# Kernel tuning notes

Hardware: AMD Instinct MI355X
Metric: run time of the kernel (lower is better)

Reference implementation:

```python
import jax, jax.numpy as jnp
import numpy as np

T, B, A_DIM = 64, 128, 5
N_AGENTS, N_CAP = 8, 7
OBS_D = 64
CAP_D = N_AGENTS * N_CAP  # 56
FC, HN, TGT = 128, 128, 64
D = N_CAP + 1  # transformer model dim = 8
NH, FF, NL = 4, 64, 2
EPS = 1e-6


def _ln(x, s, b):
    m = jnp.mean(x, -1, keepdims=True)
    v = jnp.mean(jnp.square(x - m), -1, keepdims=True)
    return (x - m) * jax.lax.rsqrt(v + EPS) * s + b


def _hyper(x, w1, b1, w2, b2):
    return jax.nn.relu(x @ w1 + b1) @ w2 + b2


def setup_inputs() -> dict:
    key = jax.random.key(0)
    ks = iter(jax.random.split(key, 40))

    def rn(shape, s=0.1):
        return jax.random.normal(next(ks), shape, jnp.float32) * s

    return dict(
        hidden=jnp.zeros((B, FC), jnp.float32),
        full_obs=jax.random.normal(next(ks), (T, B, OBS_D + CAP_D), jnp.float32),
        dones=jax.random.randint(next(ks), (T, B), 0, 2, jnp.int32),
        embed_w=rn((OBS_D, FC)), embed_b=jnp.zeros((FC,), jnp.float32),
        gru_wi=rn((FC, 3 * FC)), gru_wh=rn((FC, 3 * FC)), gru_bh=jnp.zeros((3 * FC,), jnp.float32),
        tWq=rn((NL, D, D), 0.3), tWk=rn((NL, D, D), 0.3), tWv=rn((NL, D, D), 0.3), tWo=rn((NL, D, D), 0.3),
        ln1_s=jnp.ones((NL, D), jnp.float32), ln1_b=jnp.zeros((NL, D), jnp.float32),
        ffw1=rn((NL, D, FF), 0.2), ffb1=jnp.zeros((NL, FF), jnp.float32),
        ffw2=rn((NL, FF, D), 0.2), ffb2=jnp.zeros((NL, D), jnp.float32),
        ln2_s=jnp.ones((NL, D), jnp.float32), ln2_b=jnp.zeros((NL, D), jnp.float32),
        hw1_1=rn((D, HN)), hb1_1=jnp.zeros((HN,), jnp.float32), hw2_1=rn((HN, FC * TGT), 0.02), hb2_1=jnp.zeros((FC * TGT,), jnp.float32),
        hw1_2=rn((D, HN)), hb1_2=jnp.zeros((HN,), jnp.float32), hw2_2=rn((HN, TGT), 0.02), hb2_2=jnp.zeros((TGT,), jnp.float32),
        hw1_3=rn((D, HN)), hb1_3=jnp.zeros((HN,), jnp.float32), hw2_3=rn((HN, TGT * A_DIM), 0.01), hb2_3=jnp.zeros((TGT * A_DIM,), jnp.float32),
        hw1_4=rn((D, HN)), hb1_4=jnp.zeros((HN,), jnp.float32), hw2_4=rn((HN, A_DIM), 0.01), hb2_4=jnp.zeros((A_DIM,), jnp.float32),
    )


def reference(hidden, full_obs, dones, embed_w, embed_b, gru_wi, gru_wh, gru_bh,
              tWq, tWk, tWv, tWo, ln1_s, ln1_b, ffw1, ffb1, ffw2, ffb2, ln2_s, ln2_b,
              hw1_1, hb1_1, hw2_1, hb2_1, hw1_2, hb1_2, hw2_2, hb2_2,
              hw1_3, hb1_3, hw2_3, hb2_3, hw1_4, hb1_4, hw2_4, hb2_4):
    obs = full_obs[:, :, :OBS_D]          # [T,B,OBS_D]
    cap = full_obs[:, :, OBS_D:]          # [T,B,CAP_D]
    emb = jax.nn.relu(obs @ embed_w + embed_b)  # [T,B,FC]
    resets = dones.astype(bool)

    # --- GRU scan over time (flax GRUCell math: input dense no bias, hidden dense with bias) ---
    def gru_step(h, xt):
        e, d = xt
        h = jnp.where(d[:, None], 0.0, h)
        gi = e @ gru_wi                   # [B, 3*FC]
        gh = h @ gru_wh + gru_bh
        ir, iz, inn = jnp.split(gi, 3, -1)
        hr, hz, hn = jnp.split(gh, 3, -1)
        r = jax.nn.sigmoid(ir + hr)
        z = jax.nn.sigmoid(iz + hz)
        n = jnp.tanh(inn + r * hn)
        hnew = (1.0 - z) * n + z * h
        return hnew, hnew

    hidden, emb_seq = jax.lax.scan(gru_step, hidden, (emb, resets))

    # --- transformer over agents dim ---
    x = cap.reshape(T * B, N_AGENTS, N_CAP)
    flag = jnp.zeros((T * B, N_AGENTS, 1), jnp.float32).at[:, 0, 0].set(1.0)
    x = jnp.concatenate([x, flag], axis=-1)   # [N, A, D]
    hd = D // NH
    scale = 1.0 / jnp.sqrt(jnp.float32(hd))
    for l in range(NL):
        q = (x @ tWq[l]).reshape(-1, N_AGENTS, NH, hd)
        k = (x @ tWk[l]).reshape(-1, N_AGENTS, NH, hd)
        v = (x @ tWv[l]).reshape(-1, N_AGENTS, NH, hd)
        att = jax.nn.softmax(jnp.einsum('nqhd,nkhd->nhqk', q, k) * scale, axis=-1)
        o = jnp.einsum('nhqk,nkhd->nqhd', att, v).reshape(-1, N_AGENTS, D) @ tWo[l]
        # original does x = norm(attn + x); x = x + dropout(x) -> doubles x
        x = 2.0 * _ln(o + x, ln1_s[l], ln1_b[l])
        ff = jax.nn.relu(x @ ffw1[l] + ffb1[l]) @ ffw2[l] + ffb2[l]
        x = 2.0 * _ln(ff + x, ln2_s[l], ln2_b[l])
    cap_repr = jnp.mean(x, axis=1).reshape(T, B, D)

    # --- hypernetworks -> per-(t,b) weights ---
    w1 = _hyper(cap_repr, hw1_1, hb1_1, hw2_1, hb2_1).reshape(T, B, FC, TGT)
    b1 = _hyper(cap_repr, hw1_2, hb1_2, hw2_2, hb2_2).reshape(T, B, 1, TGT)
    w2 = _hyper(cap_repr, hw1_3, hb1_3, hw2_3, hb2_3).reshape(T, B, TGT, A_DIM)
    b2 = _hyper(cap_repr, hw1_4, hb1_4, hw2_4, hb2_4).reshape(T, B, 1, A_DIM)

    h1 = jax.nn.relu(emb_seq[:, :, None, :] @ w1 + b1)   # [T,B,1,TGT]
    logits = (h1 @ w2 + b2).squeeze(2)                    # [T,B,A_DIM]
    return hidden, logits
```

## Files before the change

### kernel.cpp

```cpp
#include <hip/hip_runtime.h>
#include <hip/hip_bf16.h>
#include <stdint.h>

#define TT 64
#define BB 128
#define OBSD 64
#define FOBS 120
#define FC 128
#define G3 384
#define NS 8192
#define DD 8
#define FF 64
#define HN 128
#define TGT 64
#define ADIM 5

typedef __attribute__((ext_vector_type(8))) short bf16x8;
typedef __attribute__((ext_vector_type(4))) float f32x4;

__device__ __forceinline__ float sigmoidf_(float x) { return 1.0f / (1.0f + __expf(-x)); }
__device__ __forceinline__ float tanhf_(float x) {
    float e = __expf(-2.0f * fabsf(x));
    float r = (1.0f - e) / (1.0f + e);
    return copysignf(r, x);
}
__device__ __forceinline__ unsigned short f2bf_rne(float x) {
    unsigned u = __float_as_uint(x);
    return (unsigned short)((u + 0x7fffu + ((u >> 16) & 1u)) >> 16);
}

__global__ __launch_bounds__(256) void k_embed(
    const float* __restrict__ fobs, const float* __restrict__ We,
    const float* __restrict__ be, float* __restrict__ emb)
{
    __shared__ float obs_t[64][68];
    __shared__ float W_t[64][128];
    int tid = threadIdx.x;
    int s0 = blockIdx.x * 64;
    {
        int rl = tid >> 4, e4 = tid & 15;
#pragma unroll
        for (int rr = 0; rr < 4; ++rr) {
            int r = rl + rr * 16;
            float4 v = *(const float4*)&fobs[(size_t)(s0 + r) * FOBS + e4 * 4];
            *(float4*)&obs_t[r][e4 * 4] = v;
        }
    }
#pragma unroll
    for (int i = 0; i < 8; ++i) {
        int idx = tid + i * 256;
        int e = idx >> 5, c4 = idx & 31;
        float4 v = *(const float4*)&We[(size_t)e * 128 + c4 * 4];
        *(float4*)&W_t[e][c4 * 4] = v;
    }
    __syncthreads();
    int c = tid & 127, half = tid >> 7;
    float acc[32];
    float bc = be[c];
#pragma unroll
    for (int k = 0; k < 32; ++k) acc[k] = bc;
#pragma unroll
    for (int e4 = 0; e4 < 16; ++e4) {
        float w0 = W_t[4 * e4 + 0][c], w1 = W_t[4 * e4 + 1][c];
        float w2 = W_t[4 * e4 + 2][c], w3 = W_t[4 * e4 + 3][c];
#pragma unroll
        for (int k = 0; k < 32; ++k) {
            float4 ov = *(const float4*)&obs_t[half * 32 + k][e4 * 4];
            acc[k] += ov.x * w0 + ov.y * w1 + ov.z * w2 + ov.w * w3;
        }
    }
#pragma unroll
    for (int k = 0; k < 32; ++k)
        emb[(size_t)(s0 + half * 32 + k) * FC + c] = fmaxf(acc[k], 0.0f);
}

__global__ __launch_bounds__(256) void k_gi(
    const float* __restrict__ emb, const float* __restrict__ Wi, float* __restrict__ gi)
{
    __shared__ float e_t[64][132];
    __shared__ float w_t[128 * 64];
    int tid = threadIdx.x;
    int st = blockIdx.x / 6, gt = blockIdx.x % 6;
    int s0 = st * 64, g0 = gt * 64;
#pragma unroll
    for (int i = 0; i < 8; ++i) {
        int idx = tid + i * 256;
        int r = idx >> 5, c4 = idx & 31;
        float4 v = *(const float4*)&emb[(size_t)(s0 + r) * FC + c4 * 4];
        *(float4*)&e_t[r][c4 * 4] = v;
    }
#pragma unroll
    for (int i = 0; i < 8; ++i) {
        int idx = tid + i * 256;
        int r = idx >> 4, g4 = idx & 15;
        float4 v = *(const float4*)&Wi[(size_t)r * G3 + g0 + g4 * 4];
        *(float4*)&w_t[r * 64 + g4 * 4] = v;
    }
    __syncthreads();
    int sb4 = (tid >> 4) * 4, ob4 = (tid & 15) * 4;
    float acc[4][4];
#pragma unroll
    for (int a = 0; a < 4; ++a)
#pragma unroll
        for (int b = 0; b < 4; ++b) acc[a][b] = 0.0f;
    for (int c4 = 0; c4 < 32; ++c4) {
        float4 e4[4], w4[4];
#pragma unroll
        for (int si = 0; si < 4; ++si) e4[si] = *(const float4*)&e_t[sb4 + si][c4 * 4];
#pragma unroll
        for (int cc = 0; cc < 4; ++cc) w4[cc] = *(const float4*)&w_t[(c4 * 4 + cc) * 64 + ob4];
#pragma unroll
        for (int si = 0; si < 4; ++si) {
            const float* ep = (const float*)&e4[si];
#pragma unroll
            for (int cc = 0; cc < 4; ++cc) {
                float ev = ep[cc];
                const float* wp = (const float*)&w4[cc];
                acc[si][0] += ev * wp[0];
                acc[si][1] += ev * wp[1];
                acc[si][2] += ev * wp[2];
                acc[si][3] += ev * wp[3];
            }
        }
    }
#pragma unroll
    for (int si = 0; si < 4; ++si) {
        float4 sv;
        sv.x = acc[si][0]; sv.y = acc[si][1]; sv.z = acc[si][2]; sv.w = acc[si][3];
        *(float4*)&gi[(size_t)(s0 + sb4 + si) * G3 + g0 + ob4] = sv;
    }
}

__global__ __launch_bounds__(256) void k_prepW(
    const float* __restrict__ W, unsigned short* __restrict__ W_swz)
{
    int fid = blockIdx.x * 256 + threadIdx.x;
    int lane = fid & 63;
    int ks = (fid >> 6) & 3;
    int j  = (fid >> 8) & 127;
    int nt = (fid >> 15);
    int col = nt * 16 + (lane & 15);
    int kbase = ks * 32 + ((lane >> 4) * 8);
    const float* src = W + ((size_t)j * 128 + kbase) * 64 + col;
    unsigned short o[8];
#pragma unroll
    for (int i = 0; i < 8; ++i) o[i] = f2bf_rne(src[(size_t)i * 64]);
    size_t slot = ((size_t)((nt * 128 + j) * 4 + ks)) * 64 + lane;
    *(uint4*)&W_swz[slot * 8] = *(const uint4*)o;
}

__global__ __launch_bounds__(512, 2) void k_gru(
    const float* __restrict__ gi, const float* __restrict__ Wh, const float* __restrict__ bh,
    const int* __restrict__ dones, const float* __restrict__ h0,
    float* __restrict__ emb_seq, unsigned short* __restrict__ embb,
    float* __restrict__ hid_out)
{
    __shared__ float h_lds[2][144];
    int b = blockIdx.x, tid = threadIdx.x;
    int c = tid >> 2, q = tid & 3;
    int posc = (c >> 5) * 36 + (c & 31);

    float W[96];
#pragma unroll
    for (int g = 0; g < 3; ++g)
#pragma unroll
        for (int i = 0; i < 32; ++i)
            W[g * 32 + i] = Wh[(size_t)(q * 32 + i) * G3 + g * 128 + c];
    float bq0 = bh[c], bq1 = bh[128 + c], bq2 = bh[256 + c];

    if (tid < 128) h_lds[0][(tid >> 5) * 36 + (tid & 31)] = h0[(size_t)b * FC + tid];

    const float* g0p = gi + ((size_t)0 * BB + b) * G3;
    const float* g1p = gi + ((size_t)1 * BB + b) * G3;
    float gc0 = g0p[c], gc1 = g0p[128 + c], gc2 = g0p[256 + c];
    float n10 = g1p[c], n11 = g1p[128 + c], n12 = g1p[256 + c];
    int dval = dones[b];
    int dn1 = dones[BB + b];
    __syncthreads();

    int cur = 0;
    for (int t = 0; t < TT; ++t) {
        int t2 = (t + 2 < TT) ? t + 2 : TT - 1;
        const float* gp2 = gi + ((size_t)t2 * BB + b) * G3;
        float p0 = gp2[c], p1 = gp2[128 + c], p2 = gp2[256 + c];
        int pd = dones[t2 * BB + b];

        float d0 = 0.f, d1 = 0.f, d2 = 0.f;
        const float* hb = &h_lds[cur][q * 36];
#pragma unroll
        for (int i4 = 0; i4 < 8; ++i4) {
            float4 h4 = *(const float4*)&hb[i4 * 4];
            const float* hp = (const float*)&h4;
#pragma unroll
            for (int e = 0; e < 4; ++e) {
                int i = i4 * 4 + e;
                d0 += W[i] * hp[e];
                d1 += W[32 + i] * hp[e];
                d2 += W[64 + i] * hp[e];
            }
        }
        d0 += __shfl_xor(d0, 1, 64); d0 += __shfl_xor(d0, 2, 64);
        d1 += __shfl_xor(d1, 1, 64); d1 += __shfl_xor(d1, 2, 64);
        d2 += __shfl_xor(d2, 1, 64); d2 += __shfl_xor(d2, 2, 64);

        float hs = dval ? 0.0f : 1.0f;
        float hold = h_lds[cur][posc];
        float r = sigmoidf_(gc0 + d0 * hs + bq0);
        float z = sigmoidf_(gc1 + d1 * hs + bq1);
        float n = tanhf_(gc2 + r * (d2 * hs + bq2));
        float hnew = (1.0f - z) * n + z * (hs * hold);

        if (q == 0) {
            h_lds[cur ^ 1][posc] = hnew;
            emb_seq[((size_t)t * BB + b) * FC + c] = hnew;
            embb[((size_t)t * BB + b) * FC + c] = f2bf_rne(hnew);
        }
        gc0 = n10; gc1 = n11; gc2 = n12;
        n10 = p0;  n11 = p1;  n12 = p2;
        dval = dn1; dn1 = pd;
        __syncthreads();
        cur ^= 1;
    }
    if (tid < 128) hid_out[(size_t)b * FC + tid] = h_lds[cur][(tid >> 5) * 36 + (tid & 31)];
}

__global__ __launch_bounds__(256) void k_attn(
    const float* __restrict__ fobs,
    const float* __restrict__ tWq, const float* __restrict__ tWk,
    const float* __restrict__ tWv, const float* __restrict__ tWo,
    const float* __restrict__ ln1s, const float* __restrict__ ln1b,
    const float* __restrict__ ffw1, const float* __restrict__ ffb1,
    const float* __restrict__ ffw2, const float* __restrict__ ffb2,
    const float* __restrict__ ln2s, const float* __restrict__ ln2b,
    float* __restrict__ cap_repr)
{
    __shared__ float wq[2][8][8], wk[2][8][8], wv[2][8][8], wo[2][8][8];
    __shared__ float l1s[2][8], l1b[2][8], l2s[2][8], l2b[2][8];
    __shared__ float f1[2][8][64], fb1[2][64];
    __shared__ float f2[2][64][8], fb2w[2][8];
    __shared__ float k_l[32][8][9], v_l[32][8][9];
    int tid = threadIdx.x;
    for (int i = tid; i < 128; i += 256) {
        ((float*)wq)[i] = tWq[i]; ((float*)wk)[i] = tWk[i];
        ((float*)wv)[i] = tWv[i]; ((float*)wo)[i] = tWo[i];
        ((float*)fb1)[i] = ffb1[i];
    }
    if (tid < 16) {
        ((float*)l1s)[tid] = ln1s[tid]; ((float*)l1b)[tid] = ln1b[tid];
        ((float*)l2s)[tid] = ln2s[tid]; ((float*)l2b)[tid] = ln2b[tid];
        ((float*)fb2w)[tid] = ffb2[tid];
    }
    for (int i = tid; i < 1024; i += 256) { ((float*)f1)[i] = ffw1[i]; ((float*)f2)[i] = ffw2[i]; }
    int sl = tid >> 3, a = tid & 7;
    int s = blockIdx.x * 32 + sl;
    float x[8];
#pragma unroll
    for (int i = 0; i < 7; ++i) x[i] = fobs[(size_t)s * FOBS + OBSD + a * 7 + i];
    x[7] = (a == 0) ? 1.0f : 0.0f;
    __syncthreads();
    for (int l = 0; l < 2; ++l) {
        float q[8], k[8], v[8];
#pragma unroll
        for (int d = 0; d < 8; ++d) { q[d] = 0.f; k[d] = 0.f; v[d] = 0.f; }
#pragma unroll
        for (int e = 0; e < 8; ++e) {
            float xe = x[e];
#pragma unroll
            for (int d = 0; d < 8; ++d) {
                q[d] += xe * wq[l][e][d];
                k[d] += xe * wk[l][e][d];
                v[d] += xe * wv[l][e][d];
            }
        }
#pragma unroll
        for (int d = 0; d < 8; ++d) { k_l[sl][a][d] = k[d]; v_l[sl][a][d] = v[d]; }
        __syncthreads();
        float o[8];
#pragma unroll
        for (int h = 0; h < 4; ++h) {
            float sc[8]; float mx = -1e30f;
#pragma unroll
            for (int ka = 0; ka < 8; ++ka) {
                float sv = (q[2 * h] * k_l[sl][ka][2 * h] + q[2 * h + 1] * k_l[sl][ka][2 * h + 1])
                           * 0.70710678118654752f;
                sc[ka] = sv; mx = fmaxf(mx, sv);
            }
            float ssum = 0.f;
#pragma unroll
            for (int ka = 0; ka < 8; ++ka) { sc[ka] = __expf(sc[ka] - mx); ssum += sc[ka]; }
            float inv = 1.0f / ssum;
            float o0 = 0.f, o1 = 0.f;
#pragma unroll
            for (int ka = 0; ka < 8; ++ka) {
                float at = sc[ka] * inv;
                o0 += at * v_l[sl][ka][2 * h];
                o1 += at * v_l[sl][ka][2 * h + 1];
            }
            o[2 * h] = o0; o[2 * h + 1] = o1;
        }
        float y[8];
#pragma unroll
        for (int e = 0; e < 8; ++e) y[e] = x[e];
#pragma unroll
        for (int d = 0; d < 8; ++d) {
            float od = o[d];
#pragma unroll
            for (int e = 0; e < 8; ++e) y[e] += od * wo[l][d][e];
        }
        {
            float m = 0.f;
#pragma unroll
            for (int e = 0; e < 8; ++e) m += y[e];
            m *= 0.125f;
            float vv = 0.f;
#pragma unroll
            for (int e = 0; e < 8; ++e) { float dd = y[e] - m; vv += dd * dd; }
            vv *= 0.125f;
            float rs = rsqrtf(vv + 1e-6f);
#pragma unroll
            for (int e = 0; e < 8; ++e)
                x[e] = 2.0f * ((y[e] - m) * rs * l1s[l][e] + l1b[l][e]);
        }
        float t1[64];
#pragma unroll
        for (int f = 0; f < 64; ++f) t1[f] = 0.f;
#pragma unroll
        for (int e = 0; e < 8; ++e) {
            float xe = x[e];
#pragma unroll
            for (int f = 0; f < 64; ++f) t1[f] += xe * f1[l][e][f];
        }
        float y2[8];
#pragma unroll
        for (int e = 0; e < 8; ++e) y2[e] = x[e] + fb2w[l][e];
#pragma unroll
        for (int f = 0; f < 64; ++f) {
            float tf = fmaxf(t1[f] + fb1[l][f], 0.0f);
#pragma unroll
            for (int e = 0; e < 8; ++e) y2[e] += tf * f2[l][f][e];
        }
        {
            float m = 0.f;
#pragma unroll
            for (int e = 0; e < 8; ++e) m += y2[e];
            m *= 0.125f;
            float vv = 0.f;
#pragma unroll
            for (int e = 0; e < 8; ++e) { float dd = y2[e] - m; vv += dd * dd; }
            vv *= 0.125f;
            float rs = rsqrtf(vv + 1e-6f);
#pragma unroll
            for (int e = 0; e < 8; ++e)
                x[e] = 2.0f * ((y2[e] - m) * rs * l2s[l][e] + l2b[l][e]);
        }
        __syncthreads();
    }
#pragma unroll
    for (int e = 0; e < 8; ++e) {
        float xv = x[e];
        xv += __shfl_xor(xv, 1, 8);
        xv += __shfl_xor(xv, 2, 8);
        xv += __shfl_xor(xv, 4, 8);
        if (a == 0) cap_repr[(size_t)s * 8 + e] = xv * 0.125f;
    }
}

__global__ __launch_bounds__(256) void k_hyper(
    const float* __restrict__ cap_repr, const float* __restrict__ emb_seq,
    const float* __restrict__ hw1_1, const float* __restrict__ hb1_1,
    const float* __restrict__ hw1_2, const float* __restrict__ hb1_2,
    const float* __restrict__ hw1_3, const float* __restrict__ hb1_3,
    const float* __restrict__ hw1_4, const float* __restrict__ hb1_4,
    const float* __restrict__ hb2_1,
    const float* __restrict__ hw2_2, const float* __restrict__ hb2_2,
    const float* __restrict__ hw2_3, const float* __restrict__ hb2_3,
    const float* __restrict__ hw2_4, const float* __restrict__ hb2_4,
    float* __restrict__ hh1g, float* __restrict__ b1eff,
    float* __restrict__ w2h, float* __restrict__ b2h)
{
    __shared__ float cr[16][8];
    __shared__ float hh[4][16][132];
    __shared__ float es[16][132];
    int tid = threadIdx.x;
    int s0 = blockIdx.x * 16;
    if (tid < 128) ((float*)cr)[tid] = cap_repr[(size_t)s0 * 8 + tid];
#pragma unroll
    for (int i = 0; i < 2; ++i) {
        int idx = tid + i * 256;
        int r = idx >> 5, c4 = idx & 31;
        float4 v = *(const float4*)&emb_seq[(size_t)(s0 + r) * FC + c4 * 4];
        *(float4*)&es[r][c4 * 4] = v;
    }
    __syncthreads();
#pragma unroll
    for (int it = 0; it < 32; ++it) {
        int idx = tid + it * 256;
        int u = idx & 127;
        int sn = (idx >> 7) & 15;
        int n = idx >> 11;
        const float* w = (n == 0) ? hw1_1 : ((n == 1) ? hw1_2 : ((n == 2) ? hw1_3 : hw1_4));
        const float* bb = (n == 0) ? hb1_1 : ((n == 1) ? hb1_2 : ((n == 2) ? hb1_3 : hb1_4));
        float acc = bb[u];
#pragma unroll
        for (int e = 0; e < 8; ++e) acc += cr[sn][e] * w[e * 128 + u];
        acc = fmaxf(acc, 0.0f);
        hh[n][sn][u] = acc;
        if (n == 0) hh1g[(size_t)(s0 + sn) * 128 + u] = acc;
    }
    __syncthreads();
#pragma unroll
    for (int it = 0; it < 4; ++it) {
        int idx = tid + it * 256;
        int o = idx & 63, sn = idx >> 6;
        float acc = hb2_2[o];
        for (int j = 0; j < 128; ++j) acc += hh[1][sn][j] * hw2_2[j * 64 + o];
        for (int c = 0; c < 128; ++c) acc += es[sn][c] * hb2_1[c * 64 + o];
        b1eff[(size_t)(s0 + sn) * 64 + o] = acc;
    }
    for (int it = 0; it < 2; ++it) {
        int oa = tid + it * 256;
        if (oa < 320) {
            float acc[16];
#pragma unroll
            for (int sn = 0; sn < 16; ++sn) acc[sn] = 0.f;
            for (int j = 0; j < 128; ++j) {
                float w = hw2_3[j * 320 + oa];
#pragma unroll
                for (int sn = 0; sn < 16; ++sn) acc[sn] += hh[2][sn][j] * w;
            }
            float bb = hb2_3[oa];
#pragma unroll
            for (int sn = 0; sn < 16; ++sn) w2h[(size_t)(s0 + sn) * 320 + oa] = acc[sn] + bb;
        }
    }
    if (tid < 80) {
        int aa = tid % 5, sn = tid / 5;
        float acc = hb2_4[aa];
        for (int j = 0; j < 128; ++j) acc += hh[3][sn][j] * hw2_4[j * 5 + aa];
        b2h[(size_t)(s0 + sn) * 5 + aa] = acc;
    }
}

__global__ __launch_bounds__(256) void k_bigmm_mfma(
    const unsigned short* __restrict__ embb, const float* __restrict__ hh1g,
    const unsigned short* __restrict__ W_swz, float* __restrict__ partials)
{
    __shared__ float hh1T[32][68];
    int tid = threadIdx.x;
    int nt = tid >> 6, lane = tid & 63;
    int mt = blockIdx.x >> 2, ksp = blockIdx.x & 3;
    int s0 = mt * 64, j0 = ksp * 32;

#pragma unroll
    for (int it = 0; it < 8; ++it) {
        int idx = tid + it * 256;
        int r = idx >> 5, jj = idx & 31;
        hh1T[jj][r] = hh1g[(size_t)(s0 + r) * 128 + j0 + jj];
    }

    bf16x8 emb_r[4][4];
    int rrow = lane & 15;
    int cbase = (lane >> 4) * 8;
#pragma unroll
    for (int rt = 0; rt < 4; ++rt)
#pragma unroll
        for (int ks = 0; ks < 4; ++ks)
            emb_r[rt][ks] = *(const bf16x8*)&embb[(size_t)(s0 + rt * 16 + rrow) * 128 + ks * 32 + cbase];

    const bf16x8* Wg = (const bf16x8*)W_swz + ((size_t)(nt * 128 + j0) * 4) * 64 + lane;
    bf16x8 bf[4][4];
#pragma unroll
    for (int s = 0; s < 4; ++s)
#pragma unroll
        for (int q = 0; q < 4; ++q) bf[s][q] = Wg[(size_t)s * 256 + q * 64];

    f32x4 acc[4];
#pragma unroll
    for (int rt = 0; rt < 4; ++rt) acc[rt] = (f32x4){0.f, 0.f, 0.f, 0.f};

    int hrow = 4 * (lane >> 4);
    __syncthreads();

    for (int jj = 0; jj < 32; jj += 4) {
#pragma unroll
        for (int s = 0; s < 4; ++s) {
            int j = jj + s;
            f32x4 P[4];
#pragma unroll
            for (int rt = 0; rt < 4; ++rt) P[rt] = (f32x4){0.f, 0.f, 0.f, 0.f};
#pragma unroll
            for (int ks = 0; ks < 4; ++ks) {
                bf16x8 b = bf[s][ks];
#pragma unroll
                for (int rt = 0; rt < 4; ++rt)
                    P[rt] = __builtin_amdgcn_mfma_f32_16x16x32_bf16(emb_r[rt][ks], b, P[rt], 0, 0, 0);
            }
            if (j + 4 < 32) {
#pragma unroll
                for (int q = 0; q < 4; ++q) bf[s][q] = Wg[(size_t)(j + 4) * 256 + q * 64];
            }
            const float* hp = &hh1T[j][hrow];
#pragma unroll
            for (int rt = 0; rt < 4; ++rt) {
                float4 h4 = *(const float4*)&hp[rt * 16];
                const float* hv = (const float*)&h4;
#pragma unroll
                for (int r = 0; r < 4; ++r) acc[rt][r] += hv[r] * P[rt][r];
            }
        }
    }
    float* pb = partials + (size_t)ksp * (NS * 64);
    int colg = nt * 16 + (lane & 15);
#pragma unroll
    for (int rt = 0; rt < 4; ++rt) {
#pragma unroll
        for (int r = 0; r < 4; ++r) {
            int rowg = s0 + rt * 16 + hrow + r;
            pb[(size_t)rowg * 64 + colg] = acc[rt][r];
        }
    }
}

__global__ __launch_bounds__(256) void k_final(
    const float* __restrict__ partials, const float* __restrict__ b1eff,
    const float* __restrict__ w2h, const float* __restrict__ b2h, float* __restrict__ out)
{
    int tid = threadIdx.x;
    int wv = tid >> 6, lane = tid & 63;
    int s = blockIdx.x * 4 + wv;
    float h1 = b1eff[(size_t)s * 64 + lane];
#pragma unroll
    for (int ks = 0; ks < 4; ++ks) h1 += partials[(size_t)ks * (NS * 64) + (size_t)s * 64 + lane];
    h1 = fmaxf(h1, 0.0f);
    float lg[5];
#pragma unroll
    for (int aa = 0; aa < 5; ++aa) lg[aa] = h1 * w2h[(size_t)s * 320 + lane * 5 + aa];
#pragma unroll
    for (int off = 32; off >= 1; off >>= 1) {
#pragma unroll
        for (int aa = 0; aa < 5; ++aa) lg[aa] += __shfl_xor(lg[aa], off, 64);
    }
    if (lane == 0) {
#pragma unroll
        for (int aa = 0; aa < 5; ++aa)
            out[16384 + (size_t)s * 5 + aa] = lg[aa] + b2h[(size_t)s * 5 + aa];
    }
}

extern "C" void kernel_launch(void* const* d_in, const int* in_sizes, int n_in,
                              void* d_out, int out_size, void* d_ws, size_t ws_size,
                              hipStream_t stream)
{
    (void)in_sizes; (void)n_in; (void)out_size; (void)ws_size;
    const float* hidden  = (const float*)d_in[0];
    const float* fobs    = (const float*)d_in[1];
    const int*   dones   = (const int*)d_in[2];
    const float* embed_w = (const float*)d_in[3];
    const float* embed_b = (const float*)d_in[4];
    const float* gru_wi  = (const float*)d_in[5];
    const float* gru_wh  = (const float*)d_in[6];
    const float* gru_bh  = (const float*)d_in[7];
    const float* tWq  = (const float*)d_in[8];
    const float* tWk  = (const float*)d_in[9];
    const float* tWv  = (const float*)d_in[10];
    const float* tWo  = (const float*)d_in[11];
    const float* ln1s = (const float*)d_in[12];
    const float* ln1b = (const float*)d_in[13];
    const float* ffw1 = (const float*)d_in[14];
    const float* ffb1 = (const float*)d_in[15];
    const float* ffw2 = (const float*)d_in[16];
    const float* ffb2 = (const float*)d_in[17];
    const float* ln2s = (const float*)d_in[18];
    const float* ln2b = (const float*)d_in[19];
    const float* hw1_1 = (const float*)d_in[20]; const float* hb1_1 = (const float*)d_in[21];
    const float* hw2_1 = (const float*)d_in[22]; const float* hb2_1 = (const float*)d_in[23];
    const float* hw1_2 = (const float*)d_in[24]; const float* hb1_2 = (const float*)d_in[25];
    const float* hw2_2 = (const float*)d_in[26]; const float* hb2_2 = (const float*)d_in[27];
    const float* hw1_3 = (const float*)d_in[28]; const float* hb1_3 = (const float*)d_in[29];
    const float* hw2_3 = (const float*)d_in[30]; const float* hb2_3 = (const float*)d_in[31];
    const float* hw1_4 = (const float*)d_in[32]; const float* hb1_4 = (const float*)d_in[33];
    const float* hw2_4 = (const float*)d_in[34]; const float* hb2_4 = (const float*)d_in[35];
    float* out = (float*)d_out;
    float* ws  = (float*)d_ws;

    float* gi      = ws;
    float* parts   = ws;
    float* emb     = gi      + 3145728;
    unsigned short* W_swz    = (unsigned short*)emb;
    unsigned short* emb_bf16 = (unsigned short*)(emb + 524288);
    float* emb_seq = emb     + 1048576;
    float* cap_rep = emb_seq + 1048576;
    float* hh1g    = cap_rep + 65536;
    float* b1eff_  = hh1g    + 1048576;
    float* w2hb    = b1eff_  + 524288;
    float* b2hb    = w2hb    + 2621440;

    k_embed<<<128, 256, 0, stream>>>(fobs, embed_w, embed_b, emb);
    k_gi<<<768, 256, 0, stream>>>(emb, gru_wi, gi);
    k_prepW<<<512, 256, 0, stream>>>(hw2_1, W_swz);
    k_gru<<<128, 512, 0, stream>>>(gi, gru_wh, gru_bh, dones, hidden, emb_seq, emb_bf16, out);
    k_attn<<<256, 256, 0, stream>>>(fobs, tWq, tWk, tWv, tWo, ln1s, ln1b,
                                    ffw1, ffb1, ffw2, ffb2, ln2s, ln2b, cap_rep);
    k_hyper<<<512, 256, 0, stream>>>(cap_rep, emb_seq,
                                     hw1_1, hb1_1, hw1_2, hb1_2, hw1_3, hb1_3, hw1_4, hb1_4,
                                     hb2_1, hw2_2, hb2_2, hw2_3, hb2_3, hw2_4, hb2_4,
                                     hh1g, b1eff_, w2hb, b2hb);
    k_bigmm_mfma<<<512, 256, 0, stream>>>(emb_bf16, hh1g, W_swz, parts);
    k_final<<<2048, 256, 0, stream>>>(parts, b1eff_, w2hb, b2hb, out);
}
```

Baseline: 463.4 us.

## Split big MFMA kernel rows across 8 waves to cut register pressure

The bf16 MFMA kernel now uses 512 threads per block, and each wave covers 32 rows of the 64-row tile instead of all 64. This halves the per-wave embedding and accumulator registers and shrinks the weight prefetch buffer from four j-steps to two. The aim is to raise occupancy and latency hiding through more resident waves. In exchange each W fragment is loaded by two waves, so global or L2 traffic for weights doubles, and each wave has less prefetch depth.

Result: faster. 441.8 us (-4.7%).

```diff
diff --git a/kernel.cpp b/kernel.cpp
--- a/kernel.cpp
+++ b/kernel.cpp
@@ -441,84 +441,101 @@
     }
 }
 
-__global__ __launch_bounds__(256) void k_bigmm_mfma(
+__global__ __launch_bounds__(512, 3) void k_bigmm_mfma(
     const unsigned short* __restrict__ embb, const float* __restrict__ hh1g,
     const unsigned short* __restrict__ W_swz, float* __restrict__ partials)
 {
     __shared__ float hh1T[32][68];
     int tid = threadIdx.x;
-    int nt = tid >> 6, lane = tid & 63;
+    int w = tid >> 6, lane = tid & 63;
+    int nt = w & 3, rh = w >> 2;
     int mt = blockIdx.x >> 2, ksp = blockIdx.x & 3;
     int s0 = mt * 64, j0 = ksp * 32;
 
 #pragma unroll
-    for (int it = 0; it < 8; ++it) {
-        int idx = tid + it * 256;
+    for (int it = 0; it < 4; ++it) {
+        int idx = tid + it * 512;
         int r = idx >> 5, jj = idx & 31;
         hh1T[jj][r] = hh1g[(size_t)(s0 + r) * 128 + j0 + jj];
     }
 
-    bf16x8 emb_r[4][4];
-    int rrow = lane & 15;
+    bf16x8 emb_r[2][4];
+    int rrow = rh * 32 + (lane & 15);
     int cbase = (lane >> 4) * 8;
 #pragma unroll
-    for (int rt = 0; rt < 4; ++rt)
+    for (int rt = 0; rt < 2; ++rt)
 #pragma unroll
         for (int ks = 0; ks < 4; ++ks)
-            emb_r[rt][ks] = *(const bf16x8*)&embb[(size_t)(s0 + rt * 16 + rrow) * 128 + ks * 32 + cbase];
+            emb_r[rt][ks] = *(const bf16x8*)&embb[(size_t)(s0 + rrow + rt * 16) * 128 + ks * 32 + cbase];
 
     const bf16x8* Wg = (const bf16x8*)W_swz + ((size_t)(nt * 128 + j0) * 4) * 64 + lane;
-    bf16x8 bf[4][4];
-#pragma unroll
-    for (int s = 0; s < 4; ++s)
-#pragma unroll
-        for (int q = 0; q < 4; ++q) bf[s][q] = Wg[(size_t)s * 256 + q * 64];
-
-    f32x4 acc[4];
-#pragma unroll
-    for (int rt = 0; rt < 4; ++rt) acc[rt] = (f32x4){0.f, 0.f, 0.f, 0.f};
-
-    int hrow = 4 * (lane >> 4);
+    bf16x8 bf0[4], bf1[4];
+#pragma unroll
+    for (int q = 0; q < 4; ++q) bf0[q] = Wg[q * 64];
+#pragma unroll
+    for (int q = 0; q < 4; ++q) bf1[q] = Wg[256 + q * 64];
+
+    f32x4 acc0 = (f32x4){0.f, 0.f, 0.f, 0.f};
+    f32x4 acc1 = (f32x4){0.f, 0.f, 0.f, 0.f};
+
+    int hrow = rh * 32 + 4 * (lane >> 4);
     __syncthreads();
 
-    for (int jj = 0; jj < 32; jj += 4) {
-#pragma unroll
-        for (int s = 0; s < 4; ++s) {
-            int j = jj + s;
-            f32x4 P[4];
-#pragma unroll
-            for (int rt = 0; rt < 4; ++rt) P[rt] = (f32x4){0.f, 0.f, 0.f, 0.f};
+    for (int jj = 0; jj < 32; jj += 2) {
+        {
+            f32x4 P0 = (f32x4){0.f, 0.f, 0.f, 0.f};
+            f32x4 P1 = (f32x4){0.f, 0.f, 0.f, 0.f};
 #pragma unroll
             for (int ks = 0; ks < 4; ++ks) {
-                bf16x8 b = bf[s][ks];
-#pragma unroll
-                for (int rt = 0; rt < 4; ++rt)
-                    P[rt] = __builtin_amdgcn_mfma_f32_16x16x32_bf16(emb_r[rt][ks], b, P[rt], 0, 0, 0);
-            }
-            if (j + 4 < 32) {
-#pragma unroll
-                for (int q = 0; q < 4; ++q) bf[s][q] = Wg[(size_t)(j + 4) * 256 + q * 64];
-            }
-            const float* hp = &hh1T[j][hrow];
-#pragma unroll
-            for (int rt = 0; rt < 4; ++rt) {
-                float4 h4 = *(const float4*)&hp[rt * 16];
-                const float* hv = (const float*)&h4;
-#pragma unroll
-                for (int r = 0; r < 4; ++r) acc[rt][r] += hv[r] * P[rt][r];
+                P0 = __builtin_amdgcn_mfma_f32_16x16x32_bf16(emb_r[0][ks], bf0[ks], P0, 0, 0, 0);
+                P1 = __builtin_amdgcn_mfma_f32_16x16x32_bf16(emb_r[1][ks], bf0[ks], P1, 0, 0, 0);
+            }
+            if (jj + 2 < 32) {
+#pragma unroll
+                for (int q = 0; q < 4; ++q) bf0[q] = Wg[(size_t)(jj + 2) * 256 + q * 64];
+            }
+            const float* hp = &hh1T[jj][hrow];
+            float4 h0 = *(const float4*)&hp[0];
+            float4 h1 = *(const float4*)&hp[16];
+            const float* h0v = (const float*)&h0;
+            const float* h1v = (const float*)&h1;
+#pragma unroll
+            for (int r = 0; r < 4; ++r) {
+                acc0[r] += h0v[r] * P0[r];
+                acc1[r] += h1v[r] * P1[r];
+            }
+        }
+        {
+            f32x4 P0 = (f32x4){0.f, 0.f, 0.f, 0.f};
+            f32x4 P1 = (f32x4){0.f, 0.f, 0.f, 0.f};
+#pragma unroll
+            for (int ks = 0; ks < 4; ++ks) {
+                P0 = __builtin_amdgcn_mfma_f32_16x16x32_bf16(emb_r[0][ks], bf1[ks], P0, 0, 0, 0);
+                P1 = __builtin_amdgcn_mfma_f32_16x16x32_bf16(emb_r[1][ks], bf1[ks], P1, 0, 0, 0);
+            }
+            if (jj + 3 < 32) {
+#pragma unroll
+                for (int q = 0; q < 4; ++q) bf1[q] = Wg[(size_t)(jj + 3) * 256 + q * 64];
+            }
+            const float* hp = &hh1T[jj + 1][hrow];
+            float4 h0 = *(const float4*)&hp[0];
+            float4 h1 = *(const float4*)&hp[16];
+            const float* h0v = (const float*)&h0;
+            const float* h1v = (const float*)&h1;
+#pragma unroll
+            for (int r = 0; r < 4; ++r) {
+                acc0[r] += h0v[r] * P0[r];
+                acc1[r] += h1v[r] * P1[r];
             }
         }
     }
     float* pb = partials + (size_t)ksp * (NS * 64);
     int colg = nt * 16 + (lane & 15);
-#pragma unroll
-    for (int rt = 0; rt < 4; ++rt) {
-#pragma unroll
-        for (int r = 0; r < 4; ++r) {
-            int rowg = s0 + rt * 16 + hrow + r;
-            pb[(size_t)rowg * 64 + colg] = acc[rt][r];
-        }
-    }
+    int rbase = s0 + rh * 32 + 4 * (lane >> 4);
+#pragma unroll
+    for (int r = 0; r < 4; ++r) pb[(size_t)(rbase + r) * 64 + colg] = acc0[r];
+#pragma unroll
+    for (int r = 0; r < 4; ++r) pb[(size_t)(rbase + 16 + r) * 64 + colg] = acc1[r];
 }
 
 __global__ __launch_bounds__(256) void k_final(
@@ -605,6 +622,6 @@
                                      hw1_1, hb1_1, hw1_2, hb1_2, hw1_3, hb1_3, hw1_4, hb1_4,
                                      hb2_1, hw2_2, hb2_2, hw2_3, hb2_3, hw2_4, hb2_4,
                                      hh1g, b1eff_, w2hb, b2hb);
-    k_bigmm_mfma<<<512, 256, 0, stream>>>(emb_bf16, hh1g, W_swz, parts);
+    k_bigmm_mfma<<<512, 512, 0, stream>>>(emb_bf16, hh1g, W_swz, parts);
     k_final<<<2048, 256, 0, stream>>>(parts, b1eff_, w2hb, b2hb, out);
 }
```
